# Kernel optimization log

Hardware: AMD Instinct MI355X
Metric: run time of the kernel (lower is better)

Reference implementation:

```python
import jax, jax.numpy as jnp
import numpy as np

N = 4096          # n_nodes
M = 8192          # m_nodes (= 2*N, required by block structure)
D = 128           # in_dim == hidden_dim (conv1 is reapplied to its own output)
H = 128
NUM_ITERS = 3


def setup_inputs() -> dict:
    key = jax.random.key(0)
    ks = jax.random.split(key, 6)
    X = jax.random.normal(ks[0], (N, D), dtype=jnp.float32)
    R = jax.random.uniform(ks[1], (N, N), dtype=jnp.float32)
    A = 0.5 * (R + R.T)  # symmetric, strictly positive connectivity matrix
    # upsample MLP: Linear(n_nodes -> m_nodes - n_nodes), torch weight layout [out, in]
    W_up = jax.random.normal(ks[2], (M - N, N), dtype=jnp.float32) * 0.02
    b_up = jnp.zeros((M - N,), dtype=jnp.float32)
    # GCNConv linear weights stored [in, out]
    W1 = jax.random.normal(ks[3], (D, H), dtype=jnp.float32) * 0.05
    b1 = jnp.zeros((H,), dtype=jnp.float32)
    W2 = jax.random.normal(ks[4], (H, H), dtype=jnp.float32) * 0.05
    b2 = jnp.zeros((H,), dtype=jnp.float32)
    return dict(X=X, A=A, W_up=W_up, b_up=b_up, W1=W1, b1=b1, W2=W2, b2=b2)


def _gcn(Adj, X, W, b):
    # PyG GCNConv on a fully dense, strictly-positive weighted graph:
    # every diagonal entry is nonzero, so add_remaining_self_loops is a no-op and
    # out = D^{-1/2} A D^{-1/2} (X W) + b  exactly.
    deg = Adj.sum(axis=0)                         # [m] column degree
    dinv = jnp.where(deg > 0, jax.lax.rsqrt(deg), 0.0)
    An = Adj * dinv[:, None] * dinv[None, :]      # symmetric normalization
    return An @ (X @ W) + b


def reference(X, A, W_up, b_up, W1, b1, W2, b2):
    # new_nodes = upsample_mlp(X.T).T  -> [M-N, D]
    new_nodes = (X.T @ W_up.T + b_up).T
    Xu = jnp.concatenate([X, new_nodes], axis=0)  # [M, D]
    # block adjacency: [[A, A.T], [A, sigmoid(new @ new.T)]]
    Adj = jnp.block([[A, A.T],
                     [A, jax.nn.sigmoid(new_nodes @ new_nodes.T)]])  # [M, M]
    A_out = Adj
    for _ in range(NUM_ITERS):
        Xu = jax.nn.relu(_gcn(Adj, Xu, W1, b1))
        Adj = jax.nn.sigmoid(Xu @ Xu.T)           # mid-loop adjacency rebuild
        Xu = jax.nn.relu(_gcn(Adj, Xu, W2, b2))
        A_out = jax.nn.sigmoid(Xu @ Xu.T)
        # NOTE: edge_index for the next conv1 is NOT rebuilt from A_out in the
        # original (only after conv1), so Adj carries the mid-loop matrix.
    return A_out
```

## Files before the change

kernel.cpp:

```cpp
#include <hip/hip_runtime.h>
#include <hip/hip_bf16.h>


#define N_NODES 4096
#define M_NODES 8192
#define DIM 128
#define SLICE_ELEMS ((size_t)M_NODES * DIM)

typedef __attribute__((ext_vector_type(4))) float f32x4;
typedef __attribute__((ext_vector_type(8))) short bf16x8;

__device__ __forceinline__ unsigned short f2bf(float f) {
  union { float f; unsigned u; } v; v.f = f;
  unsigned r = v.u + 0x7fffu + ((v.u >> 16) & 1u);
  return (unsigned short)(r >> 16);
}

__device__ __forceinline__ void gld16(unsigned short* lds, const unsigned short* g) {
  __builtin_amdgcn_global_load_lds(
      (const __attribute__((address_space(1))) unsigned int*)g,
      (__attribute__((address_space(3))) unsigned int*)lds, 16, 0, 0);
}

__device__ __forceinline__ float sigmoidf_(float x) { return 1.0f / (1.0f + __expf(-x)); }


__global__ void cast_x_kernel(const float* __restrict__ X, unsigned short* __restrict__ Xu,
                              unsigned short* __restrict__ XT,
                              float* __restrict__ colsumA) {
  int idx = blockIdx.x * 256 + threadIdx.x;
  if (idx < N_NODES) colsumA[idx] = 0.f;
  int i = idx >> 7, c = idx & 127;
  unsigned short b = f2bf(X[idx]);
  Xu[idx] = b;
  XT[(size_t)c * N_NODES + i] = b;
}

__global__ void cast_wt2_kernel(const float* __restrict__ W1, const float* __restrict__ W2,
                                unsigned short* __restrict__ WT1,
                                unsigned short* __restrict__ WT2) {
  int idx = blockIdx.x * 256 + threadIdx.x;
  const float* W = idx < 16384 ? W1 : W2;
  unsigned short* WT = idx < 16384 ? WT1 : WT2;
  int j = idx & 16383;
  int k = j >> 7, c = j & 127;
  WT[c * DIM + k] = f2bf(W[j]);
}

__global__ void cast_a_kernel(const float* __restrict__ A, unsigned short* __restrict__ Adj,
                              float* __restrict__ colsumA) {
  int c = blockIdx.x * 256 + threadIdx.x;
  int r0 = blockIdx.y * 128;
  int tm = r0 >> 7;
  int kc = c >> 10, st = (c & 1023) >> 5, e = c & 31;
  size_t a1 = ((size_t)(tm)      * 8 + kc)     * 131072 + (size_t)st * 4096 + e;
  size_t a2 = ((size_t)(tm)      * 8 + 4 + kc) * 131072 + (size_t)st * 4096 + e;
  size_t a3 = ((size_t)(tm + 32) * 8 + kc)     * 131072 + (size_t)st * 4096 + e;
  float s = 0.f;
  for (int r = 0; r < 128; ++r) {
    float a = A[(size_t)(r0 + r) * N_NODES + c];
    unsigned short b = f2bf(a);
    Adj[a1 + r * 32] = b; Adj[a2 + r * 32] = b; Adj[a3 + r * 32] = b;
    s += a;
  }
  atomicAdd(&colsumA[c], s);
}

__global__ void init_deg_kernel(const float* __restrict__ colsumA, float* __restrict__ deg) {
  int i = blockIdx.x * 256 + threadIdx.x;
  deg[i] = (i < N_NODES) ? 2.0f * colsumA[i] : colsumA[i - N_NODES];
}


__global__ __launch_bounds__(256, 2)
void agg64_kernel(const unsigned short* __restrict__ At,
                  const unsigned short* __restrict__ BT, long ldb,
                  float* __restrict__ accBase, int kIters) {
  __shared__ __align__(16) unsigned short smem[18432];
  const int t = threadIdx.x, w = t >> 6, lane = t & 63;
  const int q = lane >> 4, l15 = lane & 15;
  const int sx = (l15 >> 1) & 3;
  const int tm = blockIdx.x >> 1;
  const int h2048 = (blockIdx.x & 1) * 2048;
  const int sg0 = blockIdx.y * kIters;
  const int arow = t >> 2;
  const int xchk = (t & 3) ^ ((t >> 3) & 3);

  auto STAGE = [&](int s, int b) {
    unsigned short* la = smem + b * 6144;
    unsigned short* lb = la + 2048;
    int sg = sg0 + s;
    size_t aaddr = ((size_t)tm * 8 + (sg >> 5)) * 131072 + (size_t)(sg & 31) * 4096 + h2048;
    gld16(&la[t * 8],        &At[aaddr + arow * 32 + xchk * 8]);
    gld16(&lb[t * 8],        &BT[(size_t)arow * ldb + (size_t)sg * 32 + xchk * 8]);
    gld16(&lb[2048 + t * 8], &BT[(size_t)(64 + arow) * ldb + (size_t)sg * 32 + xchk * 8]);
  };

  f32x4 acc[8];
#pragma unroll
  for (int b = 0; b < 8; ++b) acc[b] = (f32x4)0.f;

  STAGE(0, 0);
  STAGE(1, 1);

  for (int s = 0; s < kIters; ++s) {
    if (s + 2 < kIters) {
      STAGE(s + 2, (s + 2) % 3);
      asm volatile("s_waitcnt vmcnt(6)" ::: "memory");
    } else if (s + 1 < kIters) {
      asm volatile("s_waitcnt vmcnt(3)" ::: "memory");
    } else {
      asm volatile("s_waitcnt vmcnt(0)" ::: "memory");
    }
    __builtin_amdgcn_s_barrier();
    __builtin_amdgcn_sched_barrier(0);

    const unsigned short* la = smem + (s % 3) * 6144;
    const unsigned short* lb = la + 2048;
    bf16x8 a0 = *(const bf16x8*)&la[(w * 16 + l15) * 32 + (q ^ sx) * 8];
#pragma unroll
    for (int nt = 0; nt < 8; ++nt) {
      bf16x8 b = *(const bf16x8*)&lb[(nt * 16 + l15) * 32 + (q ^ sx) * 8];
      acc[nt] = __builtin_amdgcn_mfma_f32_16x16x32_bf16(a0, b, acc[nt], 0, 0, 0);
    }
    __builtin_amdgcn_sched_barrier(0);
    __builtin_amdgcn_s_barrier();
    __builtin_amdgcn_sched_barrier(0);
  }
  float* ct = accBase + (size_t)blockIdx.y * SLICE_ELEMS + (size_t)blockIdx.x * 8192;
#pragma unroll
  for (int nt = 0; nt < 8; ++nt)
    *(f32x4*)&ct[((w * 8 + nt) * 256) + (q * 16 + l15) * 4] = acc[nt];
}


__global__ __launch_bounds__(256)
void up_agg_f32(const float* __restrict__ Wup, const unsigned short* __restrict__ BT,
                float* __restrict__ accBase) {
  __shared__ __align__(16) unsigned short smem[6144];
  unsigned short* la = smem;
  unsigned short* lb = smem + 2048;
  const int t = threadIdx.x, w = t >> 6, lane = t & 63;
  const int q = lane >> 4, l15 = lane & 15;
  const int r0 = blockIdx.x * 64;
  const int k0 = blockIdx.y * 512;
  const int arow = t >> 2, achk = t & 3;

  f32x4 acc[8];
#pragma unroll
  for (int b = 0; b < 8; ++b) acc[b] = (f32x4)0.f;

  for (int s = 0; s < 16; ++s) {
    int kb = k0 + s * 32;
    __syncthreads();
    gld16(&lb[t * 8],        &BT[(size_t)arow * N_NODES + kb + achk * 8]);
    gld16(&lb[2048 + t * 8], &BT[(size_t)(64 + arow) * N_NODES + kb + achk * 8]);
    const float* ap = &Wup[(size_t)(r0 + (t >> 2)) * N_NODES + kb + (t & 3) * 8];
    float4 v0 = *(const float4*)ap;
    float4 v1 = *(const float4*)(ap + 4);
    ushort4 o0, o1;
    o0.x = f2bf(v0.x); o0.y = f2bf(v0.y); o0.z = f2bf(v0.z); o0.w = f2bf(v0.w);
    o1.x = f2bf(v1.x); o1.y = f2bf(v1.y); o1.z = f2bf(v1.z); o1.w = f2bf(v1.w);
    *(ushort4*)&la[t * 8] = o0;
    *(ushort4*)&la[t * 8 + 4] = o1;
    __syncthreads();

    bf16x8 a0 = *(const bf16x8*)&la[(w * 16 + l15) * 32 + q * 8];
#pragma unroll
    for (int nt = 0; nt < 8; ++nt) {
      bf16x8 b = *(const bf16x8*)&lb[(nt * 16 + l15) * 32 + q * 8];
      acc[nt] = __builtin_amdgcn_mfma_f32_16x16x32_bf16(a0, b, acc[nt], 0, 0, 0);
    }
  }
  float* ct = accBase + (size_t)blockIdx.y * SLICE_ELEMS + (size_t)blockIdx.x * 8192;
#pragma unroll
  for (int nt = 0; nt < 8; ++nt)
    *(f32x4*)&ct[((w * 8 + nt) * 256) + (q * 16 + l15) * 4] = acc[nt];
}

__global__ void reduce64_kernel(const float* __restrict__ acc,
                                unsigned short* __restrict__ dst,
                                const float* __restrict__ bias_row,
                                const float* __restrict__ bias_col,
                                const float* __restrict__ deg, int mode, int nSlices) {
  int p = blockIdx.x * 256 + threadIdx.x;
  float s = 0.f;
  for (int sp = 0; sp < nSlices; ++sp) s += acc[(size_t)sp * SLICE_ELEMS + p];
  int tile = p >> 13, r = p & 8191;
  int grp = r >> 8;
  int w = grp >> 3, nt = grp & 7;
  int r2 = r & 255;
  int i = r2 & 3, ql = r2 >> 2;
  int row = tile * 64 + w * 16 + (ql >> 4) * 4 + i;
  int col = nt * 16 + (ql & 15);
  float v;
  if (mode == 0) {
    v = s + bias_row[row];
  } else {
    float d = deg[row];
    float dv = d > 0.f ? rsqrtf(d) : 0.f;
    v = fmaxf(dv * s + bias_col[col], 0.f);
  }
  dst[(size_t)row * DIM + col] = f2bf(v);
}


template <int MODE>
__global__ __launch_bounds__(256)
void rebuild_kernel(const unsigned short* __restrict__ XA,
                    const unsigned short* __restrict__ XB,
                    void* __restrict__ out, long p1 ,
                    long col0, float* __restrict__ deg, int nB) {
  __shared__ __align__(16) unsigned short smem[34816];
  __shared__ float lcol[128];
  __shared__ float lrow[128];
  unsigned short* lA = smem;
  unsigned short* lB = smem + 16384;
  const int t = threadIdx.x, w = t >> 6, lane = t & 63;
  const int q = lane >> 4, l15 = lane & 15;
  const int sx = (l15 >> 1) & 3;

  int rem = blockIdx.x, bi = 0;
  while (rem >= nB - bi) { rem -= nB - bi; ++bi; }
  const int bj = bi + rem;
  const int i0 = bi * 128, j0 = bj * 128;
  const bool offdiag = (bi != bj);

  const int srow = t >> 2;
  const int xchk = (t & 3) ^ ((t >> 3) & 3);
#pragma unroll
  for (int kk = 0; kk < 4; ++kk)
#pragma unroll
    for (int h = 0; h < 2; ++h) {
      gld16(&lA[kk * 4096 + h * 2048 + t * 8],
            &XA[(size_t)(i0 + h * 64 + srow) * DIM + kk * 32 + xchk * 8]);
      gld16(&lB[kk * 4096 + h * 2048 + t * 8],
            &XB[(size_t)(j0 + h * 64 + srow) * DIM + kk * 32 + xchk * 8]);
    }
  if (MODE == 0 && t < 128) { lcol[t] = 0.f; lrow[t] = 0.f; }
  __syncthreads();

  f32x4 acc[2][8];
#pragma unroll
  for (int a = 0; a < 2; ++a)
#pragma unroll
    for (int b = 0; b < 8; ++b) acc[a][b] = (f32x4)0.f;

#pragma unroll
  for (int kk = 0; kk < 4; ++kk) {
    bf16x8 a0 = *(const bf16x8*)&lA[kk * 4096 + (w * 32 + l15) * 32 + ((q ^ sx)) * 8];
    bf16x8 a1 = *(const bf16x8*)&lA[kk * 4096 + (w * 32 + 16 + l15) * 32 + ((q ^ sx)) * 8];
#pragma unroll
    for (int nt = 0; nt < 8; ++nt) {
      bf16x8 b = *(const bf16x8*)&lB[kk * 4096 + (nt * 16 + l15) * 32 + ((q ^ sx)) * 8];
      acc[0][nt] = __builtin_amdgcn_mfma_f32_16x16x32_bf16(a0, b, acc[0][nt], 0, 0, 0);
      acc[1][nt] = __builtin_amdgcn_mfma_f32_16x16x32_bf16(a1, b, acc[1][nt], 0, 0, 0);
    }
  }
  __syncthreads();

  if (MODE == 0) {
    unsigned short* lC  = smem;
    unsigned short* lCt = smem + 17408;
    float rs[2][4] = {{0.f, 0.f, 0.f, 0.f}, {0.f, 0.f, 0.f, 0.f}};
#pragma unroll
    for (int mt = 0; mt < 2; ++mt)
#pragma unroll
      for (int nt = 0; nt < 8; ++nt) {
        float cs = 0.f;
#pragma unroll
        for (int i = 0; i < 4; ++i) {
          float sv = sigmoidf_(acc[mt][nt][i]);
          cs += sv;
          unsigned short hb = f2bf(sv);
          int row = w * 32 + mt * 16 + q * 4 + i, colL = nt * 16 + l15;
          lC[row * 136 + colL] = hb;
          if (offdiag) { lCt[colL * 136 + row] = hb; rs[mt][i] += sv; }
        }
        cs += __shfl_xor(cs, 16);
        cs += __shfl_xor(cs, 32);
        if (lane < 16) atomicAdd(&lcol[nt * 16 + lane], cs);
      }
    if (offdiag) {
#pragma unroll
      for (int mt = 0; mt < 2; ++mt)
#pragma unroll
        for (int i = 0; i < 4; ++i) {
          float v = rs[mt][i];
          v += __shfl_xor(v, 1); v += __shfl_xor(v, 2);
          v += __shfl_xor(v, 4); v += __shfl_xor(v, 8);
          if (l15 == 0) atomicAdd(&lrow[w * 32 + mt * 16 + q * 4 + i], v);
        }
    }
    __syncthreads();
    unsigned short* og = (unsigned short*)out;
    {
      const long rowbase = p1 + i0, colbase = col0 + j0;
      const size_t tb = ((size_t)(rowbase >> 7) * 8 + (colbase >> 10)) * 131072;
      const int stb = (int)((colbase & 1023) >> 5);
#pragma unroll
      for (int cc = 0; cc < 8; ++cc) {
        int ch = t + cc * 256;
        int row = ch >> 4, c16 = ch & 15;
        *(bf16x8*)&og[tb + (size_t)(stb + (c16 >> 2)) * 4096 + row * 32 + (c16 & 3) * 8] =
            *(const bf16x8*)&lC[row * 136 + c16 * 8];
      }
    }
    if (offdiag) {
      const long rowbase = p1 + j0, colbase = col0 + i0;
      const size_t tb = ((size_t)(rowbase >> 7) * 8 + (colbase >> 10)) * 131072;
      const int stb = (int)((colbase & 1023) >> 5);
#pragma unroll
      for (int cc = 0; cc < 8; ++cc) {
        int ch = t + cc * 256;
        int row = ch >> 4, c16 = ch & 15;
        *(bf16x8*)&og[tb + (size_t)(stb + (c16 >> 2)) * 4096 + row * 32 + (c16 & 3) * 8] =
            *(const bf16x8*)&lCt[row * 136 + c16 * 8];
      }
    }
    if (t < 128) atomicAdd(&deg[col0 + j0 + t], lcol[t]);
    if (offdiag && t < 128) atomicAdd(&deg[col0 + i0 + t], lrow[t]);
  } else {
    float* og = (float*)out;
    float* lCf = (float*)smem;
#pragma unroll
    for (int mt = 0; mt < 2; ++mt)
#pragma unroll
      for (int nt = 0; nt < 8; ++nt)
#pragma unroll
        for (int i = 0; i < 4; ++i) acc[mt][nt][i] = sigmoidf_(acc[mt][nt][i]);
#pragma unroll
    for (int h2 = 0; h2 < 2; ++h2) {
      __syncthreads();
      if ((w >> 1) == h2) {
#pragma unroll
        for (int mt = 0; mt < 2; ++mt)
#pragma unroll
          for (int nt = 0; nt < 8; ++nt)
#pragma unroll
            for (int i = 0; i < 4; ++i)
              lCf[((w & 1) * 32 + mt * 16 + q * 4 + i) * 132 + nt * 16 + l15] =
                  acc[mt][nt][i];
      }
      __syncthreads();
#pragma unroll
      for (int j = 0; j < 8; ++j) {
        int ch = t + j * 256;
        int r64 = ch >> 5, c4 = (ch & 31) * 4;
        *(f32x4*)&og[(size_t)(i0 + h2 * 64 + r64) * p1 + j0 + c4] =
            *(const f32x4*)&lCf[r64 * 132 + c4];
      }
    }
    if (offdiag) {
#pragma unroll
      for (int h2 = 0; h2 < 2; ++h2) {
        __syncthreads();
#pragma unroll
        for (int mt = 0; mt < 2; ++mt)
#pragma unroll
          for (int nt = 0; nt < 8; ++nt)
            if ((nt >> 2) == h2) {
#pragma unroll
              for (int i = 0; i < 4; ++i)
                lCf[((nt & 3) * 16 + l15) * 132 + (w * 32 + mt * 16 + q * 4 + i)] =
                    acc[mt][nt][i];
            }
        __syncthreads();
#pragma unroll
        for (int j = 0; j < 8; ++j) {
          int ch = t + j * 256;
          int r64 = ch >> 5, c4 = (ch & 31) * 4;
          *(f32x4*)&og[(size_t)(j0 + h2 * 64 + r64) * p1 + i0 + c4] =
              *(const f32x4*)&lCf[r64 * 132 + c4];
        }
      }
    }
  }
}


__global__ __launch_bounds__(256)
void yz_kernel(const unsigned short* __restrict__ Xu, const unsigned short* __restrict__ WT,
               const float* __restrict__ deg, unsigned short* __restrict__ ZT, int ldz,
               float* __restrict__ zbuf) {
  __shared__ __align__(16) unsigned short smem[32768];
  unsigned short* lA = smem;
  unsigned short* lB = smem + 16384;
  const int t = threadIdx.x, w = t >> 6, lane = t & 63;
  const int q = lane >> 4, l15 = lane & 15;
  const int sx = (l15 >> 1) & 3;
  const int r0 = blockIdx.x * 128;
  if (zbuf) {
    int gid = blockIdx.x * 256 + t;
    if (gid < M_NODES) zbuf[gid] = 0.f;
  }
  const int srow = t >> 2;
  const int xchk = (t & 3) ^ ((t >> 3) & 3);
#pragma unroll
  for (int kk = 0; kk < 4; ++kk)
#pragma unroll
    for (int h = 0; h < 2; ++h) {
      gld16(&lA[kk * 4096 + h * 2048 + t * 8],
            &Xu[(size_t)(r0 + h * 64 + srow) * DIM + kk * 32 + xchk * 8]);
      gld16(&lB[kk * 4096 + h * 2048 + t * 8],
            &WT[(size_t)(h * 64 + srow) * DIM + kk * 32 + xchk * 8]);
    }
  __syncthreads();

  f32x4 acc[2][8];
#pragma unroll
  for (int a = 0; a < 2; ++a)
#pragma unroll
    for (int b = 0; b < 8; ++b) acc[a][b] = (f32x4)0.f;

#pragma unroll
  for (int kk = 0; kk < 4; ++kk) {
    bf16x8 a0 = *(const bf16x8*)&lA[kk * 4096 + (w * 32 + l15) * 32 + (q ^ sx) * 8];
    bf16x8 a1 = *(const bf16x8*)&lA[kk * 4096 + (w * 32 + 16 + l15) * 32 + (q ^ sx) * 8];
#pragma unroll
    for (int nt = 0; nt < 8; ++nt) {
      bf16x8 b = *(const bf16x8*)&lB[kk * 4096 + (nt * 16 + l15) * 32 + (q ^ sx) * 8];
      acc[0][nt] = __builtin_amdgcn_mfma_f32_16x16x32_bf16(a0, b, acc[0][nt], 0, 0, 0);
      acc[1][nt] = __builtin_amdgcn_mfma_f32_16x16x32_bf16(a1, b, acc[1][nt], 0, 0, 0);
    }
  }
  __syncthreads();
  unsigned short* lT = smem;
#pragma unroll
  for (int mt = 0; mt < 2; ++mt)
#pragma unroll
    for (int i = 0; i < 4; ++i) {
      int r = w * 32 + mt * 16 + q * 4 + i;
      float d = deg[r0 + r];
      float dv = d > 0.f ? rsqrtf(d) : 0.f;
#pragma unroll
      for (int nt = 0; nt < 8; ++nt)
        lT[(nt * 16 + l15) * 136 + r] = f2bf(dv * acc[mt][nt][i]);
    }
  __syncthreads();
#pragma unroll
  for (int cc = 0; cc < 8; ++cc) {
    int ch = t + cc * 256;
    int c = ch >> 4, c16 = ch & 15;
    *(bf16x8*)&ZT[(size_t)c * ldz + r0 + c16 * 8] = *(const bf16x8*)&lT[c * 136 + c16 * 8];
  }
}


extern "C" void kernel_launch(void* const* d_in, const int* in_sizes, int n_in,
                              void* d_out, int out_size, void* d_ws, size_t ws_size,
                              hipStream_t stream) {
  (void)in_sizes; (void)n_in; (void)out_size;
  const float* X   = (const float*)d_in[0];
  const float* A   = (const float*)d_in[1];
  const float* Wup = (const float*)d_in[2];
  const float* bup = (const float*)d_in[3];
  const float* W1  = (const float*)d_in[4];
  const float* b1  = (const float*)d_in[5];
  const float* W2  = (const float*)d_in[6];
  const float* b2  = (const float*)d_in[7];

  const size_t ADJ_BYTES = (size_t)M_NODES * M_NODES * 2;
  char* ws = (char*)d_ws;
  size_t off = 0;
  auto alloc = [&](size_t bytes) {
    char* p = ws + off;
    off += (bytes + 255) & ~(size_t)255;
    return p;
  };
  float*          accb    = (float*)alloc(8 * SLICE_ELEMS * 4);
  unsigned short* Xu      = (unsigned short*)alloc((size_t)M_NODES * DIM * 2);
  unsigned short* ZT      = (unsigned short*)alloc((size_t)DIM * M_NODES * 2);
  unsigned short* XT      = (unsigned short*)alloc((size_t)DIM * N_NODES * 2);
  unsigned short* W1T     = (unsigned short*)alloc(DIM * DIM * 2);
  unsigned short* W2T     = (unsigned short*)alloc(DIM * DIM * 2);
  float*          colsumA = (float*)alloc(N_NODES * 4);
  float*          degA    = (float*)alloc(M_NODES * 4);
  float*          degB    = (float*)alloc(M_NODES * 4);

  unsigned short* Adj;
  if (ws_size >= off + ADJ_BYTES) Adj = (unsigned short*)(ws + off);
  else                            Adj = (unsigned short*)d_out;

  unsigned short* XuNew = Xu + (size_t)N_NODES * DIM;

  cast_x_kernel<<<N_NODES * DIM / 256, 256, 0, stream>>>(X, Xu, XT, colsumA);
  cast_wt2_kernel<<<128, 256, 0, stream>>>(W1, W2, W1T, W2T);

  up_agg_f32<<<dim3(N_NODES / 64, 8), 256, 0, stream>>>(Wup, XT, accb);
  reduce64_kernel<<<N_NODES * DIM / 256, 256, 0, stream>>>(
      accb, XuNew, bup, nullptr, nullptr, 0, 8);

  cast_a_kernel<<<dim3(N_NODES / 256, N_NODES / 128), 256, 0, stream>>>(A, Adj, colsumA);
  init_deg_kernel<<<M_NODES / 256, 256, 0, stream>>>(colsumA, degA);
  rebuild_kernel<0><<<32 * 33 / 2, 256, 0, stream>>>(
      XuNew, XuNew, Adj, N_NODES, N_NODES, degA, 32);

  float* degCur = degA;
  float* degMid = degB;
  for (int it = 0; it < 3; ++it) {
    yz_kernel<<<M_NODES / 128, 256, 0, stream>>>(Xu, W1T, degCur, ZT, M_NODES, degMid);
    agg64_kernel<<<dim3(M_NODES / 64, 4), 256, 0, stream>>>(Adj, ZT, M_NODES, accb, 64);
    reduce64_kernel<<<M_NODES * DIM / 256, 256, 0, stream>>>(
        accb, Xu, nullptr, b1, degCur, 1, 4);
    rebuild_kernel<0><<<64 * 65 / 2, 256, 0, stream>>>(
        Xu, Xu, Adj, 0, 0, degMid, 64);
    yz_kernel<<<M_NODES / 128, 256, 0, stream>>>(Xu, W2T, degMid, ZT, M_NODES, nullptr);
    agg64_kernel<<<dim3(M_NODES / 64, 4), 256, 0, stream>>>(Adj, ZT, M_NODES, accb, 64);
    reduce64_kernel<<<M_NODES * DIM / 256, 256, 0, stream>>>(
        accb, Xu, nullptr, b2, degMid, 1, 4);
    if (it == 2)
      rebuild_kernel<1><<<64 * 65 / 2, 256, 0, stream>>>(
          Xu, Xu, d_out, M_NODES, 0, nullptr, 64);
    float* tmp = degCur; degCur = degMid; degMid = tmp;
  }
}
```

Measured before the change: 908.4 us.

## Replace split-K aggregation plus reduce with full-K fused epilogue kernel

The aggregation GEMM (normalized adjacency times Z) now runs the full K=8192 reduction inside one block per 32 output rows, with a 5-stage LDS pipeline and a fused degree-scale, bias and ReLU epilogue that writes bf16 directly. This removes the fp32 partial-sum slices and the separate reduce kernel in the main loop. The yz kernel is retiled to 64 rows per block with a new XOR swizzle. The trade-off is fewer blocks (256) with one block per CU and smaller output tiles, so each block streams Z more times and occupancy drops.

```diff
diff --git a/kernel.cpp b/kernel.cpp
--- a/kernel.cpp
+++ b/kernel.cpp
@@ -72,65 +72,92 @@
 }
 
 
-__global__ __launch_bounds__(256, 2)
-void agg64_kernel(const unsigned short* __restrict__ At,
-                  const unsigned short* __restrict__ BT, long ldb,
-                  float* __restrict__ accBase, int kIters) {
-  __shared__ __align__(16) unsigned short smem[18432];
+__global__ __launch_bounds__(256, 1)
+void agg_full(const unsigned short* __restrict__ At,
+              const unsigned short* __restrict__ BT, long ldb,
+              unsigned short* __restrict__ Xout,
+              const float* __restrict__ bias_col,
+              const float* __restrict__ deg) {
+  __shared__ __align__(16) unsigned short smem[51200];
   const int t = threadIdx.x, w = t >> 6, lane = t & 63;
   const int q = lane >> 4, l15 = lane & 15;
-  const int sx = (l15 >> 1) & 3;
-  const int tm = blockIdx.x >> 1;
-  const int h2048 = (blockIdx.x & 1) * 2048;
-  const int sg0 = blockIdx.y * kIters;
-  const int arow = t >> 2;
-  const int xchk = (t & 3) ^ ((t >> 3) & 3);
+  const int ms = w & 1, nh = w >> 1;
+  const int r0 = blockIdx.x * 32;
+  const int tm = blockIdx.x >> 2;
+  const int rr = (blockIdx.x & 3) * 32 + (t >> 3);
+  const int cA = (t & 7) ^ ((t >> 3) & 7);
+  const int sgAdd = cA >> 2;
+  const int koffA = (cA & 3) * 8;
 
   auto STAGE = [&](int s, int b) {
-    unsigned short* la = smem + b * 6144;
+    unsigned short* la = smem + b * 10240;
     unsigned short* lb = la + 2048;
-    int sg = sg0 + s;
-    size_t aaddr = ((size_t)tm * 8 + (sg >> 5)) * 131072 + (size_t)(sg & 31) * 4096 + h2048;
-    gld16(&la[t * 8],        &At[aaddr + arow * 32 + xchk * 8]);
-    gld16(&lb[t * 8],        &BT[(size_t)arow * ldb + (size_t)sg * 32 + xchk * 8]);
-    gld16(&lb[2048 + t * 8], &BT[(size_t)(64 + arow) * ldb + (size_t)sg * 32 + xchk * 8]);
+    int sg = 2 * s + sgAdd;
+    gld16(&la[t * 8],
+          &At[((size_t)tm * 8 + (sg >> 5)) * 131072 + (size_t)(sg & 31) * 4096 + rr * 32 + koffA]);
+#pragma unroll
+    for (int j = 0; j < 4; ++j) {
+      int ch = j * 256 + t;
+      int n = ch >> 3, phys = ch & 7;
+      int c = phys ^ (n & 7);
+      gld16(&lb[ch * 8], &BT[(size_t)n * ldb + (size_t)s * 64 + c * 8]);
+    }
   };
 
-  f32x4 acc[8];
-#pragma unroll
-  for (int b = 0; b < 8; ++b) acc[b] = (f32x4)0.f;
-
-  STAGE(0, 0);
-  STAGE(1, 1);
-
-  for (int s = 0; s < kIters; ++s) {
-    if (s + 2 < kIters) {
-      STAGE(s + 2, (s + 2) % 3);
-      asm volatile("s_waitcnt vmcnt(6)" ::: "memory");
-    } else if (s + 1 < kIters) {
-      asm volatile("s_waitcnt vmcnt(3)" ::: "memory");
+  f32x4 acc[4];
+#pragma unroll
+  for (int b = 0; b < 4; ++b) acc[b] = (f32x4)0.f;
+
+  STAGE(0, 0); STAGE(1, 1); STAGE(2, 2); STAGE(3, 3);
+
+  int cur = 0, nxt = 4;
+  for (int s = 0; s < 128; ++s) {
+    if (s + 4 < 128) {
+      STAGE(s + 4, nxt);
+      nxt = (nxt == 4) ? 0 : nxt + 1;
+      asm volatile("s_waitcnt vmcnt(20)" ::: "memory");
+    } else if (s + 3 < 128) {
+      asm volatile("s_waitcnt vmcnt(15)" ::: "memory");
+    } else if (s + 2 < 128) {
+      asm volatile("s_waitcnt vmcnt(10)" ::: "memory");
+    } else if (s + 1 < 128) {
+      asm volatile("s_waitcnt vmcnt(5)" ::: "memory");
     } else {
       asm volatile("s_waitcnt vmcnt(0)" ::: "memory");
     }
     __builtin_amdgcn_s_barrier();
     __builtin_amdgcn_sched_barrier(0);
 
-    const unsigned short* la = smem + (s % 3) * 6144;
+    const unsigned short* la = smem + cur * 10240;
     const unsigned short* lb = la + 2048;
-    bf16x8 a0 = *(const bf16x8*)&la[(w * 16 + l15) * 32 + (q ^ sx) * 8];
-#pragma unroll
-    for (int nt = 0; nt < 8; ++nt) {
-      bf16x8 b = *(const bf16x8*)&lb[(nt * 16 + l15) * 32 + (q ^ sx) * 8];
-      acc[nt] = __builtin_amdgcn_mfma_f32_16x16x32_bf16(a0, b, acc[nt], 0, 0, 0);
+    const int xk = (l15 & 7);
+#pragma unroll
+    for (int ks = 0; ks < 2; ++ks) {
+      bf16x8 a0 = *(const bf16x8*)&la[(ms * 16 + l15) * 64 + ((ks * 4 + q) ^ xk) * 8];
+#pragma unroll
+      for (int nt = 0; nt < 4; ++nt) {
+        int n = nh * 64 + nt * 16 + l15;
+        bf16x8 b = *(const bf16x8*)&lb[n * 64 + ((ks * 4 + q) ^ xk) * 8];
+        acc[nt] = __builtin_amdgcn_mfma_f32_16x16x32_bf16(a0, b, acc[nt], 0, 0, 0);
+      }
     }
     __builtin_amdgcn_sched_barrier(0);
     __builtin_amdgcn_s_barrier();
     __builtin_amdgcn_sched_barrier(0);
-  }
-  float* ct = accBase + (size_t)blockIdx.y * SLICE_ELEMS + (size_t)blockIdx.x * 8192;
-#pragma unroll
-  for (int nt = 0; nt < 8; ++nt)
-    *(f32x4*)&ct[((w * 8 + nt) * 256) + (q * 16 + l15) * 4] = acc[nt];
+    cur = (cur == 4) ? 0 : cur + 1;
+  }
+
+#pragma unroll
+  for (int i = 0; i < 4; ++i) {
+    int row = r0 + ms * 16 + q * 4 + i;
+    float d = deg[row];
+    float dv = d > 0.f ? rsqrtf(d) : 0.f;
+#pragma unroll
+    for (int nt = 0; nt < 4; ++nt) {
+      int col = nh * 64 + nt * 16 + l15;
+      Xout[(size_t)row * DIM + col] = f2bf(fmaxf(dv * acc[nt][i] + bias_col[col], 0.f));
+    }
+  }
 }
 
 
@@ -180,9 +207,7 @@
 
 __global__ void reduce64_kernel(const float* __restrict__ acc,
                                 unsigned short* __restrict__ dst,
-                                const float* __restrict__ bias_row,
-                                const float* __restrict__ bias_col,
-                                const float* __restrict__ deg, int mode, int nSlices) {
+                                const float* __restrict__ bias_row, int nSlices) {
   int p = blockIdx.x * 256 + threadIdx.x;
   float s = 0.f;
   for (int sp = 0; sp < nSlices; ++sp) s += acc[(size_t)sp * SLICE_ELEMS + p];
@@ -193,15 +218,7 @@
   int i = r2 & 3, ql = r2 >> 2;
   int row = tile * 64 + w * 16 + (ql >> 4) * 4 + i;
   int col = nt * 16 + (ql & 15);
-  float v;
-  if (mode == 0) {
-    v = s + bias_row[row];
-  } else {
-    float d = deg[row];
-    float dv = d > 0.f ? rsqrtf(d) : 0.f;
-    v = fmaxf(dv * s + bias_col[col], 0.f);
-  }
-  dst[(size_t)row * DIM + col] = f2bf(v);
+  dst[(size_t)row * DIM + col] = f2bf(s + bias_row[row]);
 }
 
 
@@ -383,66 +400,60 @@
 void yz_kernel(const unsigned short* __restrict__ Xu, const unsigned short* __restrict__ WT,
                const float* __restrict__ deg, unsigned short* __restrict__ ZT, int ldz,
                float* __restrict__ zbuf) {
-  __shared__ __align__(16) unsigned short smem[32768];
+  __shared__ __align__(16) unsigned short smem[24576];
   unsigned short* lA = smem;
-  unsigned short* lB = smem + 16384;
+  unsigned short* lB = smem + 8192;
   const int t = threadIdx.x, w = t >> 6, lane = t & 63;
   const int q = lane >> 4, l15 = lane & 15;
-  const int sx = (l15 >> 1) & 3;
-  const int r0 = blockIdx.x * 128;
-  if (zbuf) {
-    int gid = blockIdx.x * 256 + t;
-    if (gid < M_NODES) zbuf[gid] = 0.f;
-  }
-  const int srow = t >> 2;
-  const int xchk = (t & 3) ^ ((t >> 3) & 3);
-#pragma unroll
-  for (int kk = 0; kk < 4; ++kk)
-#pragma unroll
-    for (int h = 0; h < 2; ++h) {
-      gld16(&lA[kk * 4096 + h * 2048 + t * 8],
-            &Xu[(size_t)(r0 + h * 64 + srow) * DIM + kk * 32 + xchk * 8]);
-      gld16(&lB[kk * 4096 + h * 2048 + t * 8],
-            &WT[(size_t)(h * 64 + srow) * DIM + kk * 32 + xchk * 8]);
-    }
+  const int r0 = blockIdx.x * 64;
+  if (zbuf && t < 64) zbuf[blockIdx.x * 64 + t] = 0.f;
+#pragma unroll
+  for (int j = 0; j < 4; ++j) {
+    int ch = j * 256 + t;
+    int row = ch >> 4, phys = ch & 15;
+    int c = phys ^ (row & 7);
+    gld16(&lA[ch * 8], &Xu[(size_t)(r0 + row) * DIM + c * 8]);
+  }
+#pragma unroll
+  for (int j = 0; j < 8; ++j) {
+    int ch = j * 256 + t;
+    int row = ch >> 4, phys = ch & 15;
+    int c = phys ^ (row & 7);
+    gld16(&lB[ch * 8], &WT[(size_t)row * DIM + c * 8]);
+  }
   __syncthreads();
 
-  f32x4 acc[2][8];
-#pragma unroll
-  for (int a = 0; a < 2; ++a)
-#pragma unroll
-    for (int b = 0; b < 8; ++b) acc[a][b] = (f32x4)0.f;
-
+  f32x4 acc[8];
+#pragma unroll
+  for (int b = 0; b < 8; ++b) acc[b] = (f32x4)0.f;
+
+  const int xk = l15 & 7;
 #pragma unroll
   for (int kk = 0; kk < 4; ++kk) {
-    bf16x8 a0 = *(const bf16x8*)&lA[kk * 4096 + (w * 32 + l15) * 32 + (q ^ sx) * 8];
-    bf16x8 a1 = *(const bf16x8*)&lA[kk * 4096 + (w * 32 + 16 + l15) * 32 + (q ^ sx) * 8];
+    bf16x8 a0 = *(const bf16x8*)&lA[(w * 16 + l15) * 128 + ((kk * 4 + q) ^ xk) * 8];
 #pragma unroll
     for (int nt = 0; nt < 8; ++nt) {
-      bf16x8 b = *(const bf16x8*)&lB[kk * 4096 + (nt * 16 + l15) * 32 + (q ^ sx) * 8];
-      acc[0][nt] = __builtin_amdgcn_mfma_f32_16x16x32_bf16(a0, b, acc[0][nt], 0, 0, 0);
-      acc[1][nt] = __builtin_amdgcn_mfma_f32_16x16x32_bf16(a1, b, acc[1][nt], 0, 0, 0);
+      bf16x8 b = *(const bf16x8*)&lB[(nt * 16 + l15) * 128 + ((kk * 4 + q) ^ xk) * 8];
+      acc[nt] = __builtin_amdgcn_mfma_f32_16x16x32_bf16(a0, b, acc[nt], 0, 0, 0);
     }
   }
   __syncthreads();
   unsigned short* lT = smem;
 #pragma unroll
-  for (int mt = 0; mt < 2; ++mt)
-#pragma unroll
-    for (int i = 0; i < 4; ++i) {
-      int r = w * 32 + mt * 16 + q * 4 + i;
-      float d = deg[r0 + r];
-      float dv = d > 0.f ? rsqrtf(d) : 0.f;
-#pragma unroll
-      for (int nt = 0; nt < 8; ++nt)
-        lT[(nt * 16 + l15) * 136 + r] = f2bf(dv * acc[mt][nt][i]);
-    }
+  for (int i = 0; i < 4; ++i) {
+    int r = w * 16 + q * 4 + i;
+    float d = deg[r0 + r];
+    float dv = d > 0.f ? rsqrtf(d) : 0.f;
+#pragma unroll
+    for (int nt = 0; nt < 8; ++nt)
+      lT[(nt * 16 + l15) * 72 + r] = f2bf(dv * acc[nt][i]);
+  }
   __syncthreads();
 #pragma unroll
-  for (int cc = 0; cc < 8; ++cc) {
-    int ch = t + cc * 256;
-    int c = ch >> 4, c16 = ch & 15;
-    *(bf16x8*)&ZT[(size_t)c * ldz + r0 + c16 * 8] = *(const bf16x8*)&lT[c * 136 + c16 * 8];
+  for (int j = 0; j < 4; ++j) {
+    int ch = t + j * 256;
+    int c = ch >> 3, chunk = ch & 7;
+    *(bf16x8*)&ZT[(size_t)c * ldz + r0 + chunk * 8] = *(const bf16x8*)&lT[c * 72 + chunk * 8];
   }
 }
 
@@ -488,8 +499,7 @@
   cast_wt2_kernel<<<128, 256, 0, stream>>>(W1, W2, W1T, W2T);
 
   up_agg_f32<<<dim3(N_NODES / 64, 8), 256, 0, stream>>>(Wup, XT, accb);
-  reduce64_kernel<<<N_NODES * DIM / 256, 256, 0, stream>>>(
-      accb, XuNew, bup, nullptr, nullptr, 0, 8);
+  reduce64_kernel<<<N_NODES * DIM / 256, 256, 0, stream>>>(accb, XuNew, bup, 8);
 
   cast_a_kernel<<<dim3(N_NODES / 256, N_NODES / 128), 256, 0, stream>>>(A, Adj, colsumA);
   init_deg_kernel<<<M_NODES / 256, 256, 0, stream>>>(colsumA, degA);
@@ -499,16 +509,12 @@
   float* degCur = degA;
   float* degMid = degB;
   for (int it = 0; it < 3; ++it) {
-    yz_kernel<<<M_NODES / 128, 256, 0, stream>>>(Xu, W1T, degCur, ZT, M_NODES, degMid);
-    agg64_kernel<<<dim3(M_NODES / 64, 4), 256, 0, stream>>>(Adj, ZT, M_NODES, accb, 64);
-    reduce64_kernel<<<M_NODES * DIM / 256, 256, 0, stream>>>(
-        accb, Xu, nullptr, b1, degCur, 1, 4);
+    yz_kernel<<<M_NODES / 64, 256, 0, stream>>>(Xu, W1T, degCur, ZT, M_NODES, degMid);
+    agg_full<<<M_NODES / 32, 256, 0, stream>>>(Adj, ZT, M_NODES, Xu, b1, degCur);
     rebuild_kernel<0><<<64 * 65 / 2, 256, 0, stream>>>(
         Xu, Xu, Adj, 0, 0, degMid, 64);
-    yz_kernel<<<M_NODES / 128, 256, 0, stream>>>(Xu, W2T, degMid, ZT, M_NODES, nullptr);
-    agg64_kernel<<<dim3(M_NODES / 64, 4), 256, 0, stream>>>(Adj, ZT, M_NODES, accb, 64);
-    reduce64_kernel<<<M_NODES * DIM / 256, 256, 0, stream>>>(
-        accb, Xu, nullptr, b2, degMid, 1, 4);
+    yz_kernel<<<M_NODES / 64, 256, 0, stream>>>(Xu, W2T, degMid, ZT, M_NODES, nullptr);
+    agg_full<<<M_NODES / 32, 256, 0, stream>>>(Adj, ZT, M_NODES, Xu, b2, degMid);
     if (it == 2)
       rebuild_kernel<1><<<64 * 65 / 2, 256, 0, stream>>>(
           Xu, Xu, d_out, M_NODES, 0, nullptr, 64);
```

Result: slower. 1.014 ms (+11.7%).
